# Performance work log

Measured on AMD Instinct MI355X. Metric: run time of the kernel, lower is better.

## Reference

```python
import jax, jax.numpy as jnp
import numpy as np

N_NODES = 100_000
N_EDGES = 1_600_000
IN_FEAT = 128
N_HEADS = 8
OUT_FEAT = 16
HF = N_HEADS * OUT_FEAT  # 128
NEG_SLOPE = 0.2


def setup_inputs() -> dict:
    key = jax.random.key(0)
    k = jax.random.split(key, 9)
    x = jax.random.normal(k[0], (N_NODES, IN_FEAT), dtype=jnp.float32)
    src = jax.random.randint(k[1], (N_EDGES,), 0, N_NODES, dtype=jnp.int64)
    dst = jax.random.randint(k[2], (N_EDGES,), 0, N_NODES, dtype=jnp.int64)
    sv = 1.0 / np.sqrt(IN_FEAT)
    sa = 1.0 / np.sqrt(HF)
    Wv = jax.random.normal(k[3], (IN_FEAT, HF), dtype=jnp.float32) * sv
    bv = jnp.zeros((HF,), dtype=jnp.float32)
    Wq = jax.random.normal(k[4], (HF, N_HEADS), dtype=jnp.float32) * sa
    bq = jnp.zeros((N_HEADS,), dtype=jnp.float32)
    Wk = jax.random.normal(k[5], (HF, N_HEADS), dtype=jnp.float32) * sa
    bk = jnp.zeros((N_HEADS,), dtype=jnp.float32)
    return {"x": x, "src": src, "dst": dst, "Wv": Wv, "bv": bv,
            "Wq": Wq, "bq": bq, "Wk": Wk, "bk": bk}


def reference(x, src, dst, Wv, bv, Wq, bq, Wk, bk):
    # Dense projections (homogeneous graph: h_src == h_dst == h)
    h = x @ Wv + bv                       # [N, H*F]
    q = h @ Wq + bq                       # [N, H]  (query, attached via dst)
    k = h @ Wk + bk                       # [N, H]  (key, attached via src)
    u = h.reshape(N_NODES, N_HEADS, OUT_FEAT)  # [N, H, F]

    # Edge scores: u_add_v('k','q') -> e_ij = k[src] + q[dst], then leaky-relu
    e = k[src] + q[dst]                   # [E, H]
    coeff = jnp.where(e >= 0, e, NEG_SLOPE * e)

    # Segment softmax over incoming edges of each destination node
    seg_max = jax.ops.segment_max(coeff, dst, num_segments=N_NODES)   # [N, H]
    ex = jnp.exp(coeff - seg_max[dst])                                # [E, H]
    denom = jax.ops.segment_sum(ex, dst, num_segments=N_NODES)       # [N, H]
    attn = ex / denom[dst]                                           # [E, H]

    # Weighted message + scatter-sum aggregate
    m = u[src] * attn[:, :, None]                                    # [E, H, F]
    v = jax.ops.segment_sum(m, dst, num_segments=N_NODES)            # [N, H, F]

    return jnp.mean(v, axis=1)                                       # [N, F]
```

## Files before the change

kernel.cpp:

```cpp
#include <hip/hip_runtime.h>
#include <hip/hip_fp16.h>

#define NFEAT 128
#define NHEADS 8
#define OUTF 16
#define NPB 256
#define MAXNB 512
#define CAP 4736

typedef _Float16 half8 __attribute__((ext_vector_type(8)));
typedef float float4v __attribute__((ext_vector_type(4)));

__global__ __launch_bounds__(256) void prep_kernel(
    const float* __restrict__ Wv, const float* __restrict__ bv,
    const float* __restrict__ Wq, const float* __restrict__ bq,
    const float* __restrict__ Wk, const float* __restrict__ bk,
    float* __restrict__ Wvq, float* __restrict__ Wvk,
    float* __restrict__ bq2, float* __restrict__ bk2)
{
    const int t = threadIdx.x;
    const int idx = blockIdx.x * 256 + t;
    const int m  = idx >> 10;
    const int j  = (idx >> 3) & 127;
    const int hd = idx & 7;
    const float* w = m ? Wk : Wq;
    float acc = 0.f;
#pragma unroll 8
    for (int c = 0; c < NFEAT; c++) acc += Wv[j * NFEAT + c] * w[c * NHEADS + hd];
    if (m) Wvk[j * NHEADS + hd] = acc;
    else   Wvq[j * NHEADS + hd] = acc;

    if (blockIdx.x == 0 && t < 16) {
        int mm = t >> 3, hh = t & 7;
        const float* ww = mm ? Wk : Wq;
        float a = mm ? bk[hh] : bq[hh];
        for (int c = 0; c < NFEAT; c++) a += bv[c] * ww[c * NHEADS + hh];
        if (mm) bk2[hh] = a;
        else    bq2[hh] = a;
    }
}

__global__ __launch_bounds__(256) void gemm_h_kernel(
    const float* __restrict__ x, const float* __restrict__ Wv,
    const float* __restrict__ bv, const float* __restrict__ Wvq,
    const float* __restrict__ Wvk, const float* __restrict__ bq2,
    const float* __restrict__ bk2, __half* __restrict__ h,
    float* __restrict__ qarr, float* __restrict__ karr, int M)
{
    __shared__ _Float16 sw[144][136];
    const int t = threadIdx.x;

    for (int i = t; i < 128 * 128; i += 256) {
        int k = i >> 7, n = i & 127;
        sw[n][k] = (_Float16)Wv[i];
    }
    for (int i = t; i < 128 * 16; i += 256) {
        int k = i >> 4, o = i & 15;
        float v = (o < 8) ? Wvq[k * 8 + o] : Wvk[k * 8 + (o - 8)];
        sw[128 + o][k] = (_Float16)v;
    }
    __syncthreads();

    const int wave = t >> 6, lane = t & 63;
    const int quad = lane >> 4, l16 = lane & 15;
    const int nstrips = (M + 15) >> 4;

    float bvv[8];
#pragma unroll
    for (int tl = 0; tl < 8; tl++) bvv[tl] = bv[tl * 16 + l16];
    const float qb = (l16 < 8) ? bq2[l16] : bk2[l16 - 8];

#pragma unroll
    for (int s = 0; s < 2; s++) {
        const int strip = blockIdx.x * 8 + wave + s * 4;
        if (strip >= nstrips) break;
        const int row0 = strip * 16;
        const int xr = row0 + l16;
        const bool ok = (xr < M);
        const float* xp = x + (size_t)xr * NFEAT + quad * 8;

        half8 af[4];
#pragma unroll
        for (int kc = 0; kc < 4; kc++) {
            float4 f0 = make_float4(0.f, 0.f, 0.f, 0.f);
            float4 f1 = make_float4(0.f, 0.f, 0.f, 0.f);
            if (ok) {
                f0 = *(const float4*)(xp + kc * 32);
                f1 = *(const float4*)(xp + kc * 32 + 4);
            }
            half8 a;
            a[0] = (_Float16)f0.x; a[1] = (_Float16)f0.y;
            a[2] = (_Float16)f0.z; a[3] = (_Float16)f0.w;
            a[4] = (_Float16)f1.x; a[5] = (_Float16)f1.y;
            a[6] = (_Float16)f1.z; a[7] = (_Float16)f1.w;
            af[kc] = a;
        }

        float4v acc[9];
#pragma unroll
        for (int tl = 0; tl < 9; tl++) acc[tl] = (float4v){0.f, 0.f, 0.f, 0.f};

#pragma unroll
        for (int kc = 0; kc < 4; kc++) {
#pragma unroll
            for (int tl = 0; tl < 9; tl++) {
                half8 b = *(const half8*)&sw[tl * 16 + l16][kc * 32 + quad * 8];
                acc[tl] = __builtin_amdgcn_mfma_f32_16x16x32_f16(af[kc], b, acc[tl], 0, 0, 0);
            }
        }

#pragma unroll
        for (int r = 0; r < 4; r++) {
            int row = row0 + quad * 4 + r;
            if (row < M) {
#pragma unroll
                for (int tl = 0; tl < 8; tl++)
                    h[(size_t)row * NFEAT + tl * 16 + l16] =
                        __float2half(acc[tl][r] + bvv[tl]);
                float qv = acc[8][r] + qb;
                if (l16 < 8) qarr[(size_t)row * NHEADS + l16] = qv;
                else         karr[(size_t)row * NHEADS + (l16 - 8)] = qv;
            }
        }
    }
}

__global__ __launch_bounds__(1024) void bin_kernel(
    const int* __restrict__ src, const int* __restrict__ dst,
    int* __restrict__ tail, int* __restrict__ bin, int E, int NB)
{
    __shared__ int lcnt[MAXNB];
    __shared__ int lbase[MAXNB];
    const int t = threadIdx.x;
    const int e0 = blockIdx.x * 8192;

    for (int i = t; i < NB; i += 1024) lcnt[i] = 0;
    __syncthreads();

    int pack[8], bkt[8], rank[8];
#pragma unroll
    for (int k = 0; k < 8; k++) {
        int e = e0 + k * 1024 + t;
        bkt[k] = -1;
        if (e < E) {
            int d = dst[e];
            pack[k] = (src[e] << 8) | (d & (NPB - 1));
            bkt[k]  = d >> 8;
            rank[k] = atomicAdd(&lcnt[bkt[k]], 1);
        }
    }
    __syncthreads();
    for (int i = t; i < NB; i += 1024)
        lbase[i] = lcnt[i] ? atomicAdd(&tail[i], lcnt[i]) : 0;
    __syncthreads();

#pragma unroll
    for (int k = 0; k < 8; k++) {
        if (bkt[k] >= 0) {
            int pos = lbase[bkt[k]] + rank[k];
            if (pos < CAP) bin[(size_t)bkt[k] * CAP + pos] = pack[k];
        }
    }
}

__global__ __launch_bounds__(1024) void bucket_build_kernel(
    const int* __restrict__ bin, const int* __restrict__ tail,
    int* __restrict__ deg, int* __restrict__ off,
    int* __restrict__ csr, int N, int NB)
{
    __shared__ int stail[MAXNB];
    __shared__ int lcnt[NPB];
    __shared__ int lcur[NPB];
    __shared__ int lcsr[CAP];

    const int b = blockIdx.x;
    const int t = threadIdx.x;

    for (int i = t; i < MAXNB; i += 1024) stail[i] = (i < NB) ? tail[i] : 0;
    if (t < NPB) lcnt[t] = 0;
    __syncthreads();

    for (int o = 1; o < MAXNB; o <<= 1) {
        int u = (t < MAXNB && t >= o) ? stail[t - o] : 0;
        __syncthreads();
        if (t < MAXNB) stail[t] += u;
        __syncthreads();
    }
    const int gbase = (b > 0) ? stail[b - 1] : 0;
    const int cnt = min(tail[b], CAP);
    const int n0 = b << 8;
    const int* mybin = bin + (size_t)b * CAP;

    for (int i = t; i < cnt; i += 1024) atomicAdd(&lcnt[mybin[i] & (NPB - 1)], 1);
    __syncthreads();

    if (t < NPB) lcur[t] = lcnt[t];
    __syncthreads();
    for (int o = 1; o < NPB; o <<= 1) {
        int u = (t < NPB && t >= o) ? lcur[t - o] : 0;
        __syncthreads();
        if (t < NPB) lcur[t] += u;
        __syncthreads();
    }
    if (t < NPB) {
        int excl = lcur[t] - lcnt[t];
        lcur[t] = excl;
        int node = n0 + t;
        if (node < N) {
            deg[node] = lcnt[t];
            off[node] = gbase + excl;
        }
    }
    __syncthreads();

    for (int i = t; i < cnt; i += 1024) {
        int p = mybin[i];
        int r = atomicAdd(&lcur[p & (NPB - 1)], 1);
        lcsr[r] = p >> 8;
    }
    __syncthreads();

    for (int i = t; i < cnt; i += 1024) csr[gbase + i] = lcsr[i];
}

__global__ __launch_bounds__(256) void agg_kernel(
    const int* __restrict__ csr, const int* __restrict__ off,
    const int* __restrict__ deg, const float* __restrict__ karr,
    const float* __restrict__ qarr, const __half* __restrict__ h,
    float* __restrict__ out, int nnodes)
{
    const int wave = threadIdx.x >> 6;
    const int lane = threadIdx.x & 63;
    const int d = blockIdx.x * 4 + wave;
    if (d >= nnodes) return;

    const int dg = deg[d];
    const int o0 = off[d];
    const int h8  = lane & 7;
    const int eg  = lane >> 4;
    const int l16 = lane & 15;
    const int hd  = l16 >> 1;
    const float q1 = qarr[d * NHEADS + h8];
    const __half* hbase = h + l16 * 8;

    __half2 acc0 = __float2half2_rn(0.f);
    __half2 acc1 = __float2half2_rn(0.f);
    __half2 acc2 = __float2half2_rn(0.f);
    __half2 acc3 = __float2half2_rn(0.f);
    float den8 = 0.f;

    for (int c0 = 0; c0 < dg; c0 += 64) {
        const int cnt = min(64, dg - c0);
        int sv = (lane < cnt) ? csr[o0 + c0 + lane] : 0;
        for (int g0 = 0; g0 < cnt; g0 += 8) {
            const int epos = g0 + (lane >> 3);
            int s8 = __shfl(sv, epos, 64);
            float p = 0.f;
            if (epos < cnt) {
                float c = karr[s8 * NHEADS + h8] + q1;
                c = fmaxf(c, 0.2f * c);
                p = __expf(c) * 0.0009765625f;
            }
            den8 += p;
            __half2 ph2 = __half2half2(__float2half(p));
            int phi = *(int*)&ph2;
#pragma unroll
            for (int i = 0; i < 2; ++i) {
                int jr  = (i << 2) + eg;
                int sl  = __shfl(sv, g0 + jr, 64);
                int pw  = __shfl(phi, (jr << 3) + hd, 64);
                __half2 pv = *(__half2*)&pw;
                float4 raw = *(const float4*)(hbase + (size_t)sl * NFEAT);
                __half2 v0 = *(__half2*)&raw.x;
                __half2 v1 = *(__half2*)&raw.y;
                __half2 v2 = *(__half2*)&raw.z;
                __half2 v3 = *(__half2*)&raw.w;
                acc0 = __hfma2(pv, v0, acc0);
                acc1 = __hfma2(pv, v1, acc1);
                acc2 = __hfma2(pv, v2, acc2);
                acc3 = __hfma2(pv, v3, acc3);
            }
        }
    }

    den8 += __shfl_xor(den8, 8, 64);
    den8 += __shfl_xor(den8, 16, 64);
    den8 += __shfl_xor(den8, 32, 64);
    float dh = __shfl(den8, hd, 64);

    float f[8];
    f[0] = __low2float(acc0); f[1] = __high2float(acc0);
    f[2] = __low2float(acc1); f[3] = __high2float(acc1);
    f[4] = __low2float(acc2); f[5] = __high2float(acc2);
    f[6] = __low2float(acc3); f[7] = __high2float(acc3);

#pragma unroll
    for (int o = 16; o <= 32; o <<= 1)
#pragma unroll
        for (int i = 0; i < 8; i++) f[i] += __shfl_xor(f[i], o, 64);

    const float inv = (dg > 0) ? 0.125f / dh : 0.f;
#pragma unroll
    for (int i = 0; i < 8; i++) f[i] *= inv;

#pragma unroll
    for (int o = 2; o <= 8; o <<= 1)
#pragma unroll
        for (int i = 0; i < 8; i++) f[i] += __shfl_xor(f[i], o, 64);

    if (lane < 2) {
        float4* o4 = (float4*)(out + (size_t)d * OUTF + lane * 8);
        o4[0] = make_float4(f[0], f[1], f[2], f[3]);
        o4[1] = make_float4(f[4], f[5], f[6], f[7]);
    }
}

extern "C" void kernel_launch(void* const* d_in, const int* in_sizes, int n_in,
                              void* d_out, int out_size, void* d_ws, size_t ws_size,
                              hipStream_t stream)
{
    const float* x   = (const float*)d_in[0];
    const int*   src = (const int*)d_in[1];
    const int*   dst = (const int*)d_in[2];
    const float* Wv  = (const float*)d_in[3];
    const float* bv  = (const float*)d_in[4];
    const float* Wq  = (const float*)d_in[5];
    const float* bq  = (const float*)d_in[6];
    const float* Wk  = (const float*)d_in[7];
    const float* bk  = (const float*)d_in[8];
    float* out = (float*)d_out;

    const int N = in_sizes[0] / NFEAT;
    const int E = in_sizes[1];
    const int NB = (N + NPB - 1) / NPB;

    __half* h   = (__half*)d_ws;
    float* qarr = (float*)d_ws + (size_t)N * (NFEAT / 2);
    float* karr = qarr + (size_t)N * NHEADS;
    int* deg    = (int*)(karr + (size_t)N * NHEADS);
    int* off    = deg + N;
    int* csr    = off + N;
    float* Wvq  = (float*)(csr + E);
    float* Wvk  = Wvq + NFEAT * NHEADS;
    float* bq2  = Wvk + NFEAT * NHEADS;
    float* bk2  = bq2 + NHEADS;
    int* tail   = (int*)(bk2 + NHEADS);
    int* bin    = tail + MAXNB;

    hipMemsetAsync(tail, 0, MAXNB * sizeof(int), stream);

    prep_kernel<<<dim3(8), dim3(256), 0, stream>>>(Wv, bv, Wq, bq, Wk, bk,
                                                   Wvq, Wvk, bq2, bk2);

    bin_kernel<<<dim3((E + 8191) / 8192), dim3(1024), 0, stream>>>(
        src, dst, tail, bin, E, NB);

    bucket_build_kernel<<<dim3(NB), dim3(1024), 0, stream>>>(
        bin, tail, deg, off, csr, N, NB);

    const int nstrips = (N + 15) / 16;
    gemm_h_kernel<<<dim3((nstrips + 7) / 8), dim3(256), 0, stream>>>(
        x, Wv, bv, Wvq, Wvk, bq2, bk2, h, qarr, karr, N);

    agg_kernel<<<dim3((N + 3) / 4), dim3(256), 0, stream>>>(
        csr, off, deg, karr, qarr, h, out, N);
}
```

Before: 237.0 us.

## Process two nodes per wave, split bucket scan, fold memset into prep

The tail memset moves into prep_kernel, which saves a separate memset launch. The global bucket prefix scan moves out of every bucket_build block into a one-block scan kernel, so build blocks no longer each repeat the scan. Bin and build kernels drop to 256-thread blocks, with bin handling 16 edges per thread. The aggregation kernel now handles two destination nodes per wave with interleaved gathers to raise memory-level parallelism. The cross-lane reduction is done in half precision, which adds a little rounding risk and one extra kernel launch.

```diff
diff --git a/kernel.cpp b/kernel.cpp
--- a/kernel.cpp
+++ b/kernel.cpp
@@ -16,10 +16,11 @@
     const float* __restrict__ Wq, const float* __restrict__ bq,
     const float* __restrict__ Wk, const float* __restrict__ bk,
     float* __restrict__ Wvq, float* __restrict__ Wvk,
-    float* __restrict__ bq2, float* __restrict__ bk2)
+    float* __restrict__ bq2, float* __restrict__ bk2, int* __restrict__ tail)
 {
     const int t = threadIdx.x;
     const int idx = blockIdx.x * 256 + t;
+    if (idx < MAXNB) tail[idx] = 0;
     const int m  = idx >> 10;
     const int j  = (idx >> 3) & 127;
     const int hd = idx & 7;
@@ -125,22 +126,22 @@
     }
 }
 
-__global__ __launch_bounds__(1024) void bin_kernel(
+__global__ __launch_bounds__(256) void bin_kernel(
     const int* __restrict__ src, const int* __restrict__ dst,
     int* __restrict__ tail, int* __restrict__ bin, int E, int NB)
 {
     __shared__ int lcnt[MAXNB];
     __shared__ int lbase[MAXNB];
     const int t = threadIdx.x;
-    const int e0 = blockIdx.x * 8192;
-
-    for (int i = t; i < NB; i += 1024) lcnt[i] = 0;
-    __syncthreads();
-
-    int pack[8], bkt[8], rank[8];
-#pragma unroll
-    for (int k = 0; k < 8; k++) {
-        int e = e0 + k * 1024 + t;
+    const int e0 = blockIdx.x * 4096;
+
+    for (int i = t; i < MAXNB; i += 256) lcnt[i] = 0;
+    __syncthreads();
+
+    int pack[16], bkt[16], rank[16];
+#pragma unroll
+    for (int k = 0; k < 16; k++) {
+        int e = e0 + k * 256 + t;
         bkt[k] = -1;
         if (e < E) {
             int d = dst[e];
@@ -150,12 +151,12 @@
         }
     }
     __syncthreads();
-    for (int i = t; i < NB; i += 1024)
+    for (int i = t; i < NB; i += 256)
         lbase[i] = lcnt[i] ? atomicAdd(&tail[i], lcnt[i]) : 0;
     __syncthreads();
 
 #pragma unroll
-    for (int k = 0; k < 8; k++) {
+    for (int k = 0; k < 16; k++) {
         if (bkt[k] >= 0) {
             int pos = lbase[bkt[k]] + rank[k];
             if (pos < CAP) bin[(size_t)bkt[k] * CAP + pos] = pack[k];
@@ -163,46 +164,53 @@
     }
 }
 
-__global__ __launch_bounds__(1024) void bucket_build_kernel(
+__global__ __launch_bounds__(512) void bucket_scan_kernel(
+    const int* __restrict__ tail, int* __restrict__ base, int NB)
+{
+    __shared__ int sd[MAXNB];
+    int t = threadIdx.x;
+    int v = (t < NB) ? tail[t] : 0;
+    sd[t] = v; __syncthreads();
+    for (int o = 1; o < MAXNB; o <<= 1) {
+        int u = (t >= o) ? sd[t - o] : 0;
+        __syncthreads();
+        sd[t] += u;
+        __syncthreads();
+    }
+    if (t < NB) base[t] = sd[t] - v;
+}
+
+__global__ __launch_bounds__(256) void bucket_build_kernel(
     const int* __restrict__ bin, const int* __restrict__ tail,
-    int* __restrict__ deg, int* __restrict__ off,
-    int* __restrict__ csr, int N, int NB)
-{
-    __shared__ int stail[MAXNB];
+    const int* __restrict__ base, int* __restrict__ deg, int* __restrict__ off,
+    int* __restrict__ csr, int N)
+{
     __shared__ int lcnt[NPB];
     __shared__ int lcur[NPB];
     __shared__ int lcsr[CAP];
 
     const int b = blockIdx.x;
     const int t = threadIdx.x;
-
-    for (int i = t; i < MAXNB; i += 1024) stail[i] = (i < NB) ? tail[i] : 0;
-    if (t < NPB) lcnt[t] = 0;
-    __syncthreads();
-
-    for (int o = 1; o < MAXNB; o <<= 1) {
-        int u = (t < MAXNB && t >= o) ? stail[t - o] : 0;
-        __syncthreads();
-        if (t < MAXNB) stail[t] += u;
-        __syncthreads();
-    }
-    const int gbase = (b > 0) ? stail[b - 1] : 0;
     const int cnt = min(tail[b], CAP);
+    const int gbase = base[b];
     const int n0 = b << 8;
     const int* mybin = bin + (size_t)b * CAP;
 
-    for (int i = t; i < cnt; i += 1024) atomicAdd(&lcnt[mybin[i] & (NPB - 1)], 1);
-    __syncthreads();
-
-    if (t < NPB) lcur[t] = lcnt[t];
+    lcnt[t] = 0;
+    __syncthreads();
+
+    for (int i = t; i < cnt; i += 256) atomicAdd(&lcnt[mybin[i] & (NPB - 1)], 1);
+    __syncthreads();
+
+    lcur[t] = lcnt[t];
     __syncthreads();
     for (int o = 1; o < NPB; o <<= 1) {
-        int u = (t < NPB && t >= o) ? lcur[t - o] : 0;
+        int u = (t >= o) ? lcur[t - o] : 0;
         __syncthreads();
-        if (t < NPB) lcur[t] += u;
+        lcur[t] += u;
         __syncthreads();
     }
-    if (t < NPB) {
+    {
         int excl = lcur[t] - lcnt[t];
         lcur[t] = excl;
         int node = n0 + t;
@@ -213,14 +221,14 @@
     }
     __syncthreads();
 
-    for (int i = t; i < cnt; i += 1024) {
+    for (int i = t; i < cnt; i += 256) {
         int p = mybin[i];
         int r = atomicAdd(&lcur[p & (NPB - 1)], 1);
         lcsr[r] = p >> 8;
     }
     __syncthreads();
 
-    for (int i = t; i < cnt; i += 1024) csr[gbase + i] = lcsr[i];
+    for (int i = t; i < cnt; i += 256) csr[gbase + i] = lcsr[i];
 }
 
 __global__ __launch_bounds__(256) void agg_kernel(
@@ -231,87 +239,149 @@
 {
     const int wave = threadIdx.x >> 6;
     const int lane = threadIdx.x & 63;
-    const int d = blockIdx.x * 4 + wave;
-    if (d >= nnodes) return;
-
-    const int dg = deg[d];
-    const int o0 = off[d];
+    const int d0 = blockIdx.x * 8 + wave * 2;
+    if (d0 >= nnodes) return;
+    const int d1 = d0 + 1;
+    const bool has1 = (d1 < nnodes);
+
+    const int dg0 = deg[d0];
+    const int dg1 = has1 ? deg[d1] : 0;
+    const int o00 = off[d0];
+    const int o01 = has1 ? off[d1] : 0;
     const int h8  = lane & 7;
     const int eg  = lane >> 4;
     const int l16 = lane & 15;
     const int hd  = l16 >> 1;
-    const float q1 = qarr[d * NHEADS + h8];
+    const float q10 = qarr[d0 * NHEADS + h8];
+    const float q11 = has1 ? qarr[d1 * NHEADS + h8] : 0.f;
     const __half* hbase = h + l16 * 8;
 
-    __half2 acc0 = __float2half2_rn(0.f);
-    __half2 acc1 = __float2half2_rn(0.f);
-    __half2 acc2 = __float2half2_rn(0.f);
-    __half2 acc3 = __float2half2_rn(0.f);
-    float den8 = 0.f;
-
-    for (int c0 = 0; c0 < dg; c0 += 64) {
-        const int cnt = min(64, dg - c0);
-        int sv = (lane < cnt) ? csr[o0 + c0 + lane] : 0;
-        for (int g0 = 0; g0 < cnt; g0 += 8) {
-            const int epos = g0 + (lane >> 3);
-            int s8 = __shfl(sv, epos, 64);
-            float p = 0.f;
-            if (epos < cnt) {
-                float c = karr[s8 * NHEADS + h8] + q1;
-                c = fmaxf(c, 0.2f * c);
-                p = __expf(c) * 0.0009765625f;
-            }
-            den8 += p;
-            __half2 ph2 = __half2half2(__float2half(p));
-            int phi = *(int*)&ph2;
-#pragma unroll
-            for (int i = 0; i < 2; ++i) {
-                int jr  = (i << 2) + eg;
-                int sl  = __shfl(sv, g0 + jr, 64);
-                int pw  = __shfl(phi, (jr << 3) + hd, 64);
-                __half2 pv = *(__half2*)&pw;
-                float4 raw = *(const float4*)(hbase + (size_t)sl * NFEAT);
-                __half2 v0 = *(__half2*)&raw.x;
-                __half2 v1 = *(__half2*)&raw.y;
-                __half2 v2 = *(__half2*)&raw.z;
-                __half2 v3 = *(__half2*)&raw.w;
-                acc0 = __hfma2(pv, v0, acc0);
-                acc1 = __hfma2(pv, v1, acc1);
-                acc2 = __hfma2(pv, v2, acc2);
-                acc3 = __hfma2(pv, v3, acc3);
-            }
-        }
-    }
-
-    den8 += __shfl_xor(den8, 8, 64);
-    den8 += __shfl_xor(den8, 16, 64);
-    den8 += __shfl_xor(den8, 32, 64);
-    float dh = __shfl(den8, hd, 64);
-
-    float f[8];
-    f[0] = __low2float(acc0); f[1] = __high2float(acc0);
-    f[2] = __low2float(acc1); f[3] = __high2float(acc1);
-    f[4] = __low2float(acc2); f[5] = __high2float(acc2);
-    f[6] = __low2float(acc3); f[7] = __high2float(acc3);
-
-#pragma unroll
-    for (int o = 16; o <= 32; o <<= 1)
-#pragma unroll
-        for (int i = 0; i < 8; i++) f[i] += __shfl_xor(f[i], o, 64);
-
-    const float inv = (dg > 0) ? 0.125f / dh : 0.f;
-#pragma unroll
-    for (int i = 0; i < 8; i++) f[i] *= inv;
+    __half2 z2 = __float2half2_rn(0.f);
+    __half2 A00 = z2, A01 = z2, A02 = z2, A03 = z2;
+    __half2 A10 = z2, A11 = z2, A12 = z2, A13 = z2;
+    float den0 = 0.f, den1 = 0.f;
+
+    const int dgmax = max(dg0, dg1);
+    for (int c0 = 0; c0 < dgmax; c0 += 64) {
+        const int cnt0 = min(64, dg0 - c0);
+        const int cnt1 = min(64, dg1 - c0);
+        int sv0 = (cnt0 > 0 && lane < cnt0) ? csr[o00 + c0 + lane] : 0;
+        int sv1 = (cnt1 > 0 && lane < cnt1) ? csr[o01 + c0 + lane] : 0;
+        const int gmax = max(cnt0, cnt1);
+        for (int g0 = 0; g0 < gmax; g0 += 8) {
+            float p0 = 0.f;
+            int phi0 = 0;
+            if (g0 < cnt0) {
+                int epos = g0 + (lane >> 3);
+                int s8 = __shfl(sv0, epos, 64);
+                if (epos < cnt0) {
+                    float c = karr[s8 * NHEADS + h8] + q10;
+                    c = fmaxf(c, 0.2f * c);
+                    p0 = __expf(c) * 0.0009765625f;
+                }
+                __half2 ph = __half2half2(__float2half(p0));
+                phi0 = *(int*)&ph;
+            }
+            float p1 = 0.f;
+            int phi1 = 0;
+            if (g0 < cnt1) {
+                int epos = g0 + (lane >> 3);
+                int s8 = __shfl(sv1, epos, 64);
+                if (epos < cnt1) {
+                    float c = karr[s8 * NHEADS + h8] + q11;
+                    c = fmaxf(c, 0.2f * c);
+                    p1 = __expf(c) * 0.0009765625f;
+                }
+                __half2 ph = __half2half2(__float2half(p1));
+                phi1 = *(int*)&ph;
+            }
+            den0 += p0;
+            den1 += p1;
+
+            if (g0 < cnt0) {
+#pragma unroll
+                for (int i = 0; i < 2; ++i) {
+                    int jr = (i << 2) + eg;
+                    int sl = __shfl(sv0, g0 + jr, 64);
+                    int pw = __shfl(phi0, (jr << 3) + hd, 64);
+                    __half2 pv = *(__half2*)&pw;
+                    float4 raw = *(const float4*)(hbase + (size_t)sl * NFEAT);
+                    A00 = __hfma2(pv, *(__half2*)&raw.x, A00);
+                    A01 = __hfma2(pv, *(__half2*)&raw.y, A01);
+                    A02 = __hfma2(pv, *(__half2*)&raw.z, A02);
+                    A03 = __hfma2(pv, *(__half2*)&raw.w, A03);
+                }
+            }
+            if (g0 < cnt1) {
+#pragma unroll
+                for (int i = 0; i < 2; ++i) {
+                    int jr = (i << 2) + eg;
+                    int sl = __shfl(sv1, g0 + jr, 64);
+                    int pw = __shfl(phi1, (jr << 3) + hd, 64);
+                    __half2 pv = *(__half2*)&pw;
+                    float4 raw = *(const float4*)(hbase + (size_t)sl * NFEAT);
+                    A10 = __hfma2(pv, *(__half2*)&raw.x, A10);
+                    A11 = __hfma2(pv, *(__half2*)&raw.y, A11);
+                    A12 = __hfma2(pv, *(__half2*)&raw.z, A12);
+                    A13 = __hfma2(pv, *(__half2*)&raw.w, A13);
+                }
+            }
+        }
+    }
+
+#pragma unroll
+    for (int o = 16; o <= 32; o <<= 1) {
+        int w;
+        w = __shfl_xor(*(int*)&A00, o, 64); A00 = __hadd2(A00, *(__half2*)&w);
+        w = __shfl_xor(*(int*)&A01, o, 64); A01 = __hadd2(A01, *(__half2*)&w);
+        w = __shfl_xor(*(int*)&A02, o, 64); A02 = __hadd2(A02, *(__half2*)&w);
+        w = __shfl_xor(*(int*)&A03, o, 64); A03 = __hadd2(A03, *(__half2*)&w);
+        w = __shfl_xor(*(int*)&A10, o, 64); A10 = __hadd2(A10, *(__half2*)&w);
+        w = __shfl_xor(*(int*)&A11, o, 64); A11 = __hadd2(A11, *(__half2*)&w);
+        w = __shfl_xor(*(int*)&A12, o, 64); A12 = __hadd2(A12, *(__half2*)&w);
+        w = __shfl_xor(*(int*)&A13, o, 64); A13 = __hadd2(A13, *(__half2*)&w);
+    }
+
+    den0 += __shfl_xor(den0, 8, 64);
+    den0 += __shfl_xor(den0, 16, 64);
+    den0 += __shfl_xor(den0, 32, 64);
+    den1 += __shfl_xor(den1, 8, 64);
+    den1 += __shfl_xor(den1, 16, 64);
+    den1 += __shfl_xor(den1, 32, 64);
+    float dh0 = __shfl(den0, hd, 64);
+    float dh1 = __shfl(den1, hd, 64);
+
+    float f0[8], f1[8];
+    f0[0] = __low2float(A00); f0[1] = __high2float(A00);
+    f0[2] = __low2float(A01); f0[3] = __high2float(A01);
+    f0[4] = __low2float(A02); f0[5] = __high2float(A02);
+    f0[6] = __low2float(A03); f0[7] = __high2float(A03);
+    f1[0] = __low2float(A10); f1[1] = __high2float(A10);
+    f1[2] = __low2float(A11); f1[3] = __high2float(A11);
+    f1[4] = __low2float(A12); f1[5] = __high2float(A12);
+    f1[6] = __low2float(A13); f1[7] = __high2float(A13);
+
+    const float inv0 = (dg0 > 0) ? 0.125f / dh0 : 0.f;
+    const float inv1 = (dg1 > 0) ? 0.125f / dh1 : 0.f;
+#pragma unroll
+    for (int i = 0; i < 8; i++) { f0[i] *= inv0; f1[i] *= inv1; }
 
 #pragma unroll
     for (int o = 2; o <= 8; o <<= 1)
 #pragma unroll
-        for (int i = 0; i < 8; i++) f[i] += __shfl_xor(f[i], o, 64);
+        for (int i = 0; i < 8; i++) {
+            f0[i] += __shfl_xor(f0[i], o, 64);
+            f1[i] += __shfl_xor(f1[i], o, 64);
+        }
 
     if (lane < 2) {
-        float4* o4 = (float4*)(out + (size_t)d * OUTF + lane * 8);
-        o4[0] = make_float4(f[0], f[1], f[2], f[3]);
-        o4[1] = make_float4(f[4], f[5], f[6], f[7]);
+        float4* o4 = (float4*)(out + (size_t)d0 * OUTF + lane * 8);
+        o4[0] = make_float4(f0[0], f0[1], f0[2], f0[3]);
+        o4[1] = make_float4(f0[4], f0[5], f0[6], f0[7]);
+    } else if (lane < 4 && has1) {
+        float4* o4 = (float4*)(out + (size_t)d1 * OUTF + (lane - 2) * 8);
+        o4[0] = make_float4(f1[0], f1[1], f1[2], f1[3]);
+        o4[1] = make_float4(f1[4], f1[5], f1[6], f1[7]);
     }
 }
 
@@ -345,23 +415,24 @@
     float* bq2  = Wvk + NFEAT * NHEADS;
     float* bk2  = bq2 + NHEADS;
     int* tail   = (int*)(bk2 + NHEADS);
-    int* bin    = tail + MAXNB;
-
-    hipMemsetAsync(tail, 0, MAXNB * sizeof(int), stream);
+    int* base   = tail + MAXNB;
+    int* bin    = base + MAXNB;
 
     prep_kernel<<<dim3(8), dim3(256), 0, stream>>>(Wv, bv, Wq, bq, Wk, bk,
-                                                   Wvq, Wvk, bq2, bk2);
-
-    bin_kernel<<<dim3((E + 8191) / 8192), dim3(1024), 0, stream>>>(
+                                                   Wvq, Wvk, bq2, bk2, tail);
+
+    bin_kernel<<<dim3((E + 4095) / 4096), dim3(256), 0, stream>>>(
         src, dst, tail, bin, E, NB);
 
-    bucket_build_kernel<<<dim3(NB), dim3(1024), 0, stream>>>(
-        bin, tail, deg, off, csr, N, NB);
+    bucket_scan_kernel<<<dim3(1), dim3(512), 0, stream>>>(tail, base, NB);
+
+    bucket_build_kernel<<<dim3(NB), dim3(256), 0, stream>>>(
+        bin, tail, base, deg, off, csr, N);
 
     const int nstrips = (N + 15) / 16;
     gemm_h_kernel<<<dim3((nstrips + 7) / 8), dim3(256), 0, stream>>>(
         x, Wv, bv, Wvq, Wvk, bq2, bk2, h, qarr, karr, N);
 
-    agg_kernel<<<dim3((N + 3) / 4), dim3(256), 0, stream>>>(
+    agg_kernel<<<dim3((N + 7) / 8), dim3(256), 0, stream>>>(
         csr, off, deg, karr, qarr, h, out, N);
 }
```

After: 249.0 us. 5.1% more time.
